# Performance work log

Measured on AMD Instinct MI355X. Metric: run time of the kernel, lower is better.

## Reference

```python
import jax, jax.numpy as jnp
import numpy as np

NE = 8192       # number of mesh elements
B = 64          # batch of density fields
AVG_DEG = 32    # neighbors per element within filter radius
NNZ = NE * AVG_DEG
NEG_SLOPE = 0.001


def setup_inputs() -> dict:
    key = jax.random.key(0)
    kx, kw, ks, ki = jax.random.split(key, 4)
    x = jax.random.normal(kx, (B, NE), dtype=jnp.float32)
    fc1_weight = jax.random.normal(kw, (NE, NE), dtype=jnp.float32) * (1.0 / np.sqrt(NE))
    # sparse weights initialized uniform(-bound, bound), bound = sqrt(2/Ne)
    bound = float(np.sqrt(2.0 / NE))
    sparse_weights = jax.random.uniform(ks, (NNZ,), dtype=jnp.float32,
                                        minval=-bound, maxval=bound)
    # static COO pattern (row, col) derived from mesh connectivity Rij < Rmin
    sparse_indices = jax.random.randint(ki, (2, NNZ), 0, NE, dtype=jnp.int64)
    return {"x": x, "fc1_weight": fc1_weight,
            "sparse_weights": sparse_weights, "sparse_indices": sparse_indices}


def reference(x, fc1_weight, sparse_weights, sparse_indices):
    # dense layer: h[b, i] = sum_k x[b, k] * W[i, k]
    h = x @ fc1_weight.T                         # [B, Ne]
    rows = sparse_indices[0]                     # [nnz]
    cols = sparse_indices[1]                     # [nnz]
    # sparse mm: out[b, j] = sum_{(i,j) in pattern} h[b, i] * w_{ij}
    contrib = h[:, rows] * sparse_weights        # [B, nnz] gather + scale
    out = jnp.zeros((x.shape[0], fc1_weight.shape[0]), dtype=h.dtype)
    out = out.at[:, cols].add(contrib)           # scatter-add over columns
    # leaky_relu, negative_slope = 0.001
    return jnp.where(out >= 0, out, NEG_SLOPE * out)
```

## Files before the change

kernel.cpp:

```cpp
#include <hip/hip_runtime.h>
#include <hip/hip_bf16.h>

#define NE 8192
#define BATCH 64
#define NNZT (NE * 32)
#define KSPLIT 4
#define KCH (NE / KSPLIT)
#define BK 128
#define NSTEP (KCH / BK)
#define TN 64

typedef float f32x2 __attribute__((ext_vector_type(2)));
typedef float f32x4 __attribute__((ext_vector_type(4)));
typedef short s16x8 __attribute__((ext_vector_type(8)));

__device__ __forceinline__ unsigned f2bf(float f) {
  unsigned u = __builtin_bit_cast(unsigned, f);
  return (u + 0x7FFFu + ((u >> 16) & 1u)) >> 16;
}

__global__ void k_convert_x(const float* __restrict__ x, unsigned short* __restrict__ xb) {
  int i = (blockIdx.x * 256 + threadIdx.x) * 4;
  float4 v = *reinterpret_cast<const float4*>(x + i);
  *reinterpret_cast<ushort4*>(xb + i) =
      make_ushort4((unsigned short)f2bf(v.x), (unsigned short)f2bf(v.y),
                   (unsigned short)f2bf(v.z), (unsigned short)f2bf(v.w));
}

__global__ void k_zero(float* __restrict__ p) {
  int i = (blockIdx.x * 256 + threadIdx.x) * 4;
  *reinterpret_cast<float4*>(p + i) = make_float4(0.f, 0.f, 0.f, 0.f);
}

__global__ __launch_bounds__(512, 4) void k_dense(const unsigned short* __restrict__ xb,
                                                  const float* __restrict__ W,
                                                  float* __restrict__ ht) {
  __shared__ __align__(16) char smem[65536];
  const int tid = threadIdx.x;
  const int wv = tid >> 6, l = tid & 63;
  const int kq = blockIdx.x & (KSPLIT - 1);
  const int i0 = (blockIdx.x >> 2) * TN;
  const int k0 = kq * KCH;

  const float* wsrc = W + (size_t)(i0 + wv * 8) * NE + k0 + l * 2;
  const unsigned short* xsrc = xb + (size_t)(wv * 8) * NE + k0 + l * 2;

  const int r16 = l & 15, q = l >> 4;
  const int wrow = (wv & 3) * 16 + r16;
  const int xrow0 = (wv >> 2) * 32 + r16;
  const int fxor = (r16 & 7) << 4;

  f32x4 acc0 = {}, acc1 = {};
  f32x2 wA[8], wB[8];
  unsigned xA[8], xB[8];

#define LOADW(WR, XR, s)                                                          \
  do {                                                                            \
    _Pragma("unroll") for (int j = 0; j < 8; ++j)                                 \
        WR[j] = *reinterpret_cast<const f32x2*>(wsrc + (size_t)j * NE + (s)*BK);  \
    _Pragma("unroll") for (int j = 0; j < 8; ++j)                                 \
        XR[j] = *reinterpret_cast<const unsigned*>(xsrc + (size_t)j * NE + (s)*BK); \
    __builtin_amdgcn_sched_barrier(0);                                            \
  } while (0)

#define STORE(WR, XR, buf)                                                        \
  do {                                                                            \
    _Pragma("unroll") for (int j = 0; j < 8; ++j) {                               \
      const int r_ = wv * 8 + j;                                                  \
      const int co_ = (l * 4) ^ ((r_ & 7) << 4);                                  \
      unsigned pw_ = f2bf(WR[j][0]) | (f2bf(WR[j][1]) << 16);                     \
      *reinterpret_cast<unsigned*>(smem + (buf)*16384 + r_ * 256 + co_) = pw_;    \
      *reinterpret_cast<unsigned*>(smem + 32768 + (buf)*16384 + r_ * 256 + co_) = XR[j]; \
    }                                                                             \
    __builtin_amdgcn_sched_barrier(0);                                            \
  } while (0)

#define COMPUTE(buf)                                                              \
  do {                                                                            \
    const char* wb_ = smem + (buf)*16384 + wrow * 256;                            \
    const char* xb0_ = smem + 32768 + (buf)*16384 + xrow0 * 256;                  \
    _Pragma("unroll") for (int ks = 0; ks < 4; ++ks) {                            \
      const int col_ = (ks * 64 + q * 16) ^ fxor;                                 \
      s16x8 bw_ = *reinterpret_cast<const s16x8*>(wb_ + col_);                    \
      s16x8 a0_ = *reinterpret_cast<const s16x8*>(xb0_ + col_);                   \
      s16x8 a1_ = *reinterpret_cast<const s16x8*>(xb0_ + 4096 + col_);            \
      acc0 = __builtin_amdgcn_mfma_f32_16x16x32_bf16(a0_, bw_, acc0, 0, 0, 0);    \
      acc1 = __builtin_amdgcn_mfma_f32_16x16x32_bf16(a1_, bw_, acc1, 0, 0, 0);    \
    }                                                                             \
    __builtin_amdgcn_sched_barrier(0);                                            \
  } while (0)

#define SBAR()                                              \
  do {                                                      \
    asm volatile("s_waitcnt lgkmcnt(0)" ::: "memory");      \
    __builtin_amdgcn_s_barrier();                           \
    __builtin_amdgcn_sched_barrier(0);                      \
  } while (0)

  LOADW(wA, xA, 0);
  LOADW(wB, xB, 1);
  STORE(wA, xA, 0);
  SBAR();

  for (int s = 0; s < NSTEP; s += 2) {
    if (s + 2 < NSTEP) LOADW(wA, xA, s + 2);
    if (s + 1 < NSTEP) STORE(wB, xB, 1);
    COMPUTE(0);
    SBAR();
    if (s + 3 < NSTEP) LOADW(wB, xB, s + 3);
    if (s + 2 < NSTEP) STORE(wA, xA, 0);
    COMPUTE(1);
    SBAR();
  }

#undef LOADW
#undef STORE
#undef COMPUTE
#undef SBAR

  float* hp = ht + (size_t)(i0 + wrow) * BATCH + (wv >> 2) * 32 + q * 4;
#pragma unroll
  for (int j = 0; j < 4; ++j) atomicAdd(hp + j, acc0[j]);
#pragma unroll
  for (int j = 0; j < 4; ++j) atomicAdd(hp + 16 + j, acc1[j]);
}

__global__ void k_scatter(const float* __restrict__ ht, const float* __restrict__ sw,
                          const int* __restrict__ rows, const int* __restrict__ cols,
                          float* __restrict__ out_t) {
  const int w = (blockIdx.x * 256 + threadIdx.x) >> 6;
  const int lane = threadIdx.x & 63;
  const int n0 = w * (NNZT / 4096);
#pragma unroll 4
  for (int n = n0; n < n0 + (NNZT / 4096); ++n) {
    const int r = rows[n];
    const int c = cols[n];
    const float wv = sw[n];
    atomicAdd(out_t + (size_t)c * BATCH + lane, ht[(size_t)r * BATCH + lane] * wv);
  }
}

__global__ void k_final(const float* __restrict__ out_t, float* __restrict__ out) {
  __shared__ float tile[64][65];
  const int t = threadIdx.x;
  const int j0 = blockIdx.x * 64;
  {
    const int jl = t >> 2, b0 = (t & 3) * 16;
    const float* src = out_t + (size_t)(j0 + jl) * BATCH + b0;
#pragma unroll
    for (int e = 0; e < 16; e += 4) {
      float4 v = *reinterpret_cast<const float4*>(src + e);
      tile[jl][b0 + e + 0] = v.x;
      tile[jl][b0 + e + 1] = v.y;
      tile[jl][b0 + e + 2] = v.z;
      tile[jl][b0 + e + 3] = v.w;
    }
  }
  __syncthreads();
  {
    const int bl = t >> 2, js = (t & 3) * 16;
    float* dst = out + (size_t)bl * NE + j0 + js;
#pragma unroll
    for (int e = 0; e < 16; e += 4) {
      float a0 = tile[js + e + 0][bl];
      float a1 = tile[js + e + 1][bl];
      float a2 = tile[js + e + 2][bl];
      float a3 = tile[js + e + 3][bl];
      float4 v;
      v.x = a0 >= 0.f ? a0 : 0.001f * a0;
      v.y = a1 >= 0.f ? a1 : 0.001f * a1;
      v.z = a2 >= 0.f ? a2 : 0.001f * a2;
      v.w = a3 >= 0.f ? a3 : 0.001f * a3;
      *reinterpret_cast<float4*>(dst + e) = v;
    }
  }
}

extern "C" void kernel_launch(void* const* d_in, const int* in_sizes, int n_in,
                              void* d_out, int out_size, void* d_ws, size_t ws_size,
                              hipStream_t stream) {
  const float* x = (const float*)d_in[0];
  const float* W = (const float*)d_in[1];
  const float* sw = (const float*)d_in[2];
  const int* idx = (const int*)d_in[3];
  float* out = (float*)d_out;

  char* ws = (char*)d_ws;
  float* ht = (float*)ws;
  float* out_t = (float*)(ws + (2 << 20));
  unsigned short* xbf = (unsigned short*)(ws + (4 << 20));

  k_convert_x<<<512, 256, 0, stream>>>(x, xbf);
  k_zero<<<1024, 256, 0, stream>>>((float*)ws);
  k_dense<<<512, 512, 0, stream>>>(xbf, W, ht);
  k_scatter<<<1024, 256, 0, stream>>>(ht, sw, idx, idx + NNZT, out_t);
  k_final<<<128, 256, 0, stream>>>(out_t, out);
}
```

Baseline: 137.4 us.

## Retile dense GEMM to 256-row tiles with 8-way K split

The dense bf16 MFMA kernel now gives each block 256 output rows over a 1024-wide K chunk with BK=64. Each wave computes a 32x64 tile with eight accumulators, so every x fragment read from shared memory is reused across more W rows. Global loads are widened to 16-byte vectors and the grid is halved to 256 blocks. The cost is more LDS per block (80KB) and more registers, which lowers occupancy to 2 blocks per CU, plus twice as many atomic adds into ht from the larger K split.

Result: slower. 166.2 us (+21.0%).

```diff
diff --git a/kernel.cpp b/kernel.cpp
--- a/kernel.cpp
+++ b/kernel.cpp
@@ -4,14 +4,15 @@
 #define NE 8192
 #define BATCH 64
 #define NNZT (NE * 32)
-#define KSPLIT 4
+#define KSPLIT 8
 #define KCH (NE / KSPLIT)
-#define BK 128
+#define BK 64
 #define NSTEP (KCH / BK)
-#define TN 64
-
-typedef float f32x2 __attribute__((ext_vector_type(2)));
+#define TN 256
+
 typedef float f32x4 __attribute__((ext_vector_type(4)));
+typedef unsigned u32x4 __attribute__((ext_vector_type(4)));
+typedef unsigned u32x2 __attribute__((ext_vector_type(2)));
 typedef short s16x8 __attribute__((ext_vector_type(8)));
 
 __device__ __forceinline__ unsigned f2bf(float f) {
@@ -32,62 +33,68 @@
   *reinterpret_cast<float4*>(p + i) = make_float4(0.f, 0.f, 0.f, 0.f);
 }
 
-__global__ __launch_bounds__(512, 4) void k_dense(const unsigned short* __restrict__ xb,
+__global__ __launch_bounds__(512, 2) void k_dense(const unsigned short* __restrict__ xb,
                                                   const float* __restrict__ W,
                                                   float* __restrict__ ht) {
-  __shared__ __align__(16) char smem[65536];
+  __shared__ __align__(16) char smem[81920];
   const int tid = threadIdx.x;
   const int wv = tid >> 6, l = tid & 63;
   const int kq = blockIdx.x & (KSPLIT - 1);
-  const int i0 = (blockIdx.x >> 2) * TN;
+  const int i0 = (blockIdx.x >> 3) * TN;
   const int k0 = kq * KCH;
 
-  const float* wsrc = W + (size_t)(i0 + wv * 8) * NE + k0 + l * 2;
-  const unsigned short* xsrc = xb + (size_t)(wv * 8) * NE + k0 + l * 2;
+  const float* wsrc = W + (size_t)(i0 + wv * 32 + (l >> 4)) * NE + k0 + (l & 15) * 4;
+  const unsigned short* xsrc = xb + (size_t)(wv * 8 + (l >> 3)) * NE + k0 + (l & 7) * 8;
 
   const int r16 = l & 15, q = l >> 4;
-  const int wrow = (wv & 3) * 16 + r16;
-  const int xrow0 = (wv >> 2) * 32 + r16;
   const int fxor = (r16 & 7) << 4;
-
-  f32x4 acc0 = {}, acc1 = {};
-  f32x2 wA[8], wB[8];
-  unsigned xA[8], xB[8];
-
-#define LOADW(WR, XR, s)                                                          \
-  do {                                                                            \
-    _Pragma("unroll") for (int j = 0; j < 8; ++j)                                 \
-        WR[j] = *reinterpret_cast<const f32x2*>(wsrc + (size_t)j * NE + (s)*BK);  \
-    _Pragma("unroll") for (int j = 0; j < 8; ++j)                                 \
-        XR[j] = *reinterpret_cast<const unsigned*>(xsrc + (size_t)j * NE + (s)*BK); \
-    __builtin_amdgcn_sched_barrier(0);                                            \
-  } while (0)
-
-#define STORE(WR, XR, buf)                                                        \
-  do {                                                                            \
-    _Pragma("unroll") for (int j = 0; j < 8; ++j) {                               \
-      const int r_ = wv * 8 + j;                                                  \
-      const int co_ = (l * 4) ^ ((r_ & 7) << 4);                                  \
-      unsigned pw_ = f2bf(WR[j][0]) | (f2bf(WR[j][1]) << 16);                     \
-      *reinterpret_cast<unsigned*>(smem + (buf)*16384 + r_ * 256 + co_) = pw_;    \
-      *reinterpret_cast<unsigned*>(smem + 32768 + (buf)*16384 + r_ * 256 + co_) = XR[j]; \
-    }                                                                             \
-    __builtin_amdgcn_sched_barrier(0);                                            \
-  } while (0)
-
-#define COMPUTE(buf)                                                              \
-  do {                                                                            \
-    const char* wb_ = smem + (buf)*16384 + wrow * 256;                            \
-    const char* xb0_ = smem + 32768 + (buf)*16384 + xrow0 * 256;                  \
-    _Pragma("unroll") for (int ks = 0; ks < 4; ++ks) {                            \
-      const int col_ = (ks * 64 + q * 16) ^ fxor;                                 \
-      s16x8 bw_ = *reinterpret_cast<const s16x8*>(wb_ + col_);                    \
-      s16x8 a0_ = *reinterpret_cast<const s16x8*>(xb0_ + col_);                   \
-      s16x8 a1_ = *reinterpret_cast<const s16x8*>(xb0_ + 4096 + col_);            \
-      acc0 = __builtin_amdgcn_mfma_f32_16x16x32_bf16(a0_, bw_, acc0, 0, 0, 0);    \
-      acc1 = __builtin_amdgcn_mfma_f32_16x16x32_bf16(a1_, bw_, acc1, 0, 0, 0);    \
-    }                                                                             \
-    __builtin_amdgcn_sched_barrier(0);                                            \
+  const int wrow0 = wv * 32 + r16;
+  const int wdr = wv * 32 + (l >> 4);
+  const int xdr = wv * 8 + (l >> 3);
+
+  f32x4 acc0[4] = {}, acc1[4] = {};
+  f32x4 wA[8], wB[8];
+  u32x4 xA, xB;
+
+#define LOADW(WR, XR, s)                                                           \
+  do {                                                                             \
+    _Pragma("unroll") for (int j = 0; j < 8; ++j)                                  \
+        WR[j] = *reinterpret_cast<const f32x4*>(wsrc + (size_t)j * 4 * NE + (s)*BK); \
+    XR = *reinterpret_cast<const u32x4*>(xsrc + (s)*BK);                           \
+    __builtin_amdgcn_sched_barrier(0);                                             \
+  } while (0)
+
+#define STORE(WR, XR, buf)                                                         \
+  do {                                                                             \
+    _Pragma("unroll") for (int j = 0; j < 8; ++j) {                                \
+      const int r_ = wdr + j * 4;                                                  \
+      const int co_ = ((l & 15) * 8) ^ ((r_ & 7) << 4);                            \
+      u32x2 pw_;                                                                   \
+      pw_[0] = f2bf(WR[j][0]) | (f2bf(WR[j][1]) << 16);                            \
+      pw_[1] = f2bf(WR[j][2]) | (f2bf(WR[j][3]) << 16);                            \
+      *reinterpret_cast<u32x2*>(smem + (buf)*32768 + r_ * 128 + co_) = pw_;        \
+    }                                                                              \
+    {                                                                              \
+      const int cx_ = ((l & 7) * 16) ^ ((xdr & 7) << 4);                           \
+      *reinterpret_cast<u32x4*>(smem + 65536 + (buf)*8192 + xdr * 128 + cx_) = XR; \
+    }                                                                              \
+    __builtin_amdgcn_sched_barrier(0);                                             \
+  } while (0)
+
+#define COMPUTE(buf)                                                               \
+  do {                                                                             \
+    _Pragma("unroll") for (int ks = 0; ks < 2; ++ks) {                             \
+      const int col_ = (ks * 64 + q * 16) ^ fxor;                                  \
+      s16x8 b0_ = *reinterpret_cast<const s16x8*>(smem + (buf)*32768 + wrow0 * 128 + col_); \
+      s16x8 b1_ = *reinterpret_cast<const s16x8*>(smem + (buf)*32768 + (wrow0 + 16) * 128 + col_); \
+      _Pragma("unroll") for (int g = 0; g < 4; ++g) {                              \
+        s16x8 a_ = *reinterpret_cast<const s16x8*>(smem + 65536 + (buf)*8192 +     \
+                                                   (g * 16 + r16) * 128 + col_);   \
+        acc0[g] = __builtin_amdgcn_mfma_f32_16x16x32_bf16(a_, b0_, acc0[g], 0, 0, 0); \
+        acc1[g] = __builtin_amdgcn_mfma_f32_16x16x32_bf16(a_, b1_, acc1[g], 0, 0, 0); \
+      }                                                                            \
+    }                                                                              \
+    __builtin_amdgcn_sched_barrier(0);                                             \
   } while (0)
 
 #define SBAR()                                              \
@@ -118,11 +125,16 @@
 #undef COMPUTE
 #undef SBAR
 
-  float* hp = ht + (size_t)(i0 + wrow) * BATCH + (wv >> 2) * 32 + q * 4;
-#pragma unroll
-  for (int j = 0; j < 4; ++j) atomicAdd(hp + j, acc0[j]);
-#pragma unroll
-  for (int j = 0; j < 4; ++j) atomicAdd(hp + 16 + j, acc1[j]);
+#pragma unroll
+  for (int g = 0; g < 4; ++g) {
+    float* hp0 = ht + (size_t)(i0 + wrow0) * BATCH + g * 16 + q * 4;
+    float* hp1 = ht + (size_t)(i0 + wrow0 + 16) * BATCH + g * 16 + q * 4;
+#pragma unroll
+    for (int j = 0; j < 4; ++j) {
+      atomicAdd(hp0 + j, acc0[g][j]);
+      atomicAdd(hp1 + j, acc1[g][j]);
+    }
+  }
 }
 
 __global__ void k_scatter(const float* __restrict__ ht, const float* __restrict__ sw,
@@ -192,7 +204,7 @@
 
   k_convert_x<<<512, 256, 0, stream>>>(x, xbf);
   k_zero<<<1024, 256, 0, stream>>>((float*)ws);
-  k_dense<<<512, 512, 0, stream>>>(xbf, W, ht);
+  k_dense<<<256, 512, 0, stream>>>(xbf, W, ht);
   k_scatter<<<1024, 256, 0, stream>>>(ht, sw, idx, idx + NNZT, out_t);
   k_final<<<128, 256, 0, stream>>>(out_t, out);
 }
```

## Shrink dense GEMM tiles to 32 rows, split K eight ways, 256-thread blocks

Applied to the files above, without the earlier changes.

Retiles the dense bf16 MFMA kernel. Each block now covers 32 output rows with 4 waves instead of 64 rows with 8 waves, the K dimension is split 8 ways instead of 4, and the K step drops from 128 to 64. This gives 2048 smaller blocks with less LDS each, aiming for more blocks per CU and better spread of the memory-bound weight streaming. The cost is more global atomic adds into h, more reloads of the x tiles, and narrower 4-byte W loads per lane.

New measurement: 165.4 us. +20.4%, slower.

```diff
diff --git a/kernel.cpp b/kernel.cpp
--- a/kernel.cpp
+++ b/kernel.cpp
@@ -4,13 +4,12 @@
 #define NE 8192
 #define BATCH 64
 #define NNZT (NE * 32)
-#define KSPLIT 4
+#define KSPLIT 8
 #define KCH (NE / KSPLIT)
-#define BK 128
+#define BK 64
 #define NSTEP (KCH / BK)
-#define TN 64
-
-typedef float f32x2 __attribute__((ext_vector_type(2)));
+#define TN 32
+
 typedef float f32x4 __attribute__((ext_vector_type(4)));
 typedef short s16x8 __attribute__((ext_vector_type(8)));
 
@@ -32,60 +31,61 @@
   *reinterpret_cast<float4*>(p + i) = make_float4(0.f, 0.f, 0.f, 0.f);
 }
 
-__global__ __launch_bounds__(512, 4) void k_dense(const unsigned short* __restrict__ xb,
+__global__ __launch_bounds__(256, 6) void k_dense(const unsigned short* __restrict__ xb,
                                                   const float* __restrict__ W,
                                                   float* __restrict__ ht) {
-  __shared__ __align__(16) char smem[65536];
+  __shared__ __align__(16) char smem[24576];
   const int tid = threadIdx.x;
   const int wv = tid >> 6, l = tid & 63;
   const int kq = blockIdx.x & (KSPLIT - 1);
-  const int i0 = (blockIdx.x >> 2) * TN;
+  const int i0 = (blockIdx.x >> 3) * TN;
   const int k0 = kq * KCH;
 
-  const float* wsrc = W + (size_t)(i0 + wv * 8) * NE + k0 + l * 2;
-  const unsigned short* xsrc = xb + (size_t)(wv * 8) * NE + k0 + l * 2;
+  const float* wsrc = W + (size_t)(i0 + wv * 8) * NE + k0 + l;
+  const unsigned short* xsrc = xb + (size_t)(wv * 16 + (l >> 5)) * NE + k0 + (l & 31) * 2;
 
   const int r16 = l & 15, q = l >> 4;
-  const int wrow = (wv & 3) * 16 + r16;
-  const int xrow0 = (wv >> 2) * 32 + r16;
   const int fxor = (r16 & 7) << 4;
 
   f32x4 acc0 = {}, acc1 = {};
-  f32x2 wA[8], wB[8];
+  float wA[8], wB[8];
   unsigned xA[8], xB[8];
 
 #define LOADW(WR, XR, s)                                                          \
   do {                                                                            \
     _Pragma("unroll") for (int j = 0; j < 8; ++j)                                 \
-        WR[j] = *reinterpret_cast<const f32x2*>(wsrc + (size_t)j * NE + (s)*BK);  \
+        WR[j] = *(wsrc + (size_t)j * NE + (s)*BK);                                \
     _Pragma("unroll") for (int j = 0; j < 8; ++j)                                 \
-        XR[j] = *reinterpret_cast<const unsigned*>(xsrc + (size_t)j * NE + (s)*BK); \
+        XR[j] = *reinterpret_cast<const unsigned*>(xsrc + (size_t)(2 * j) * NE + (s)*BK); \
     __builtin_amdgcn_sched_barrier(0);                                            \
   } while (0)
 
 #define STORE(WR, XR, buf)                                                        \
   do {                                                                            \
     _Pragma("unroll") for (int j = 0; j < 8; ++j) {                               \
-      const int r_ = wv * 8 + j;                                                  \
-      const int co_ = (l * 4) ^ ((r_ & 7) << 4);                                  \
-      unsigned pw_ = f2bf(WR[j][0]) | (f2bf(WR[j][1]) << 16);                     \
-      *reinterpret_cast<unsigned*>(smem + (buf)*16384 + r_ * 256 + co_) = pw_;    \
-      *reinterpret_cast<unsigned*>(smem + 32768 + (buf)*16384 + r_ * 256 + co_) = XR[j]; \
+      const int rw_ = wv * 8 + j;                                                 \
+      const int co_ = (l * 2) ^ ((rw_ & 7) << 4);                                 \
+      *reinterpret_cast<unsigned short*>(smem + (buf)*4096 + rw_ * 128 + co_) =   \
+          (unsigned short)f2bf(WR[j]);                                            \
+    }                                                                             \
+    _Pragma("unroll") for (int j = 0; j < 8; ++j) {                               \
+      const int rx_ = wv * 16 + 2 * j + (l >> 5);                                 \
+      const int cx_ = ((l & 31) * 4) ^ ((rx_ & 7) << 4);                          \
+      *reinterpret_cast<unsigned*>(smem + 8192 + (buf)*8192 + rx_ * 128 + cx_) = XR[j]; \
     }                                                                             \
     __builtin_amdgcn_sched_barrier(0);                                            \
   } while (0)
 
 #define COMPUTE(buf)                                                              \
   do {                                                                            \
-    const char* wb_ = smem + (buf)*16384 + wrow * 256;                            \
-    const char* xb0_ = smem + 32768 + (buf)*16384 + xrow0 * 256;                  \
-    _Pragma("unroll") for (int ks = 0; ks < 4; ++ks) {                            \
+    _Pragma("unroll") for (int ks = 0; ks < 2; ++ks) {                            \
       const int col_ = (ks * 64 + q * 16) ^ fxor;                                 \
-      s16x8 bw_ = *reinterpret_cast<const s16x8*>(wb_ + col_);                    \
-      s16x8 a0_ = *reinterpret_cast<const s16x8*>(xb0_ + col_);                   \
-      s16x8 a1_ = *reinterpret_cast<const s16x8*>(xb0_ + 4096 + col_);            \
-      acc0 = __builtin_amdgcn_mfma_f32_16x16x32_bf16(a0_, bw_, acc0, 0, 0, 0);    \
-      acc1 = __builtin_amdgcn_mfma_f32_16x16x32_bf16(a1_, bw_, acc1, 0, 0, 0);    \
+      s16x8 b0_ = *reinterpret_cast<const s16x8*>(smem + (buf)*4096 + r16 * 128 + col_); \
+      s16x8 b1_ = *reinterpret_cast<const s16x8*>(smem + (buf)*4096 + (16 + r16) * 128 + col_); \
+      s16x8 a_ = *reinterpret_cast<const s16x8*>(smem + 8192 + (buf)*8192 +       \
+                                                 (wv * 16 + r16) * 128 + col_);   \
+      acc0 = __builtin_amdgcn_mfma_f32_16x16x32_bf16(a_, b0_, acc0, 0, 0, 0);     \
+      acc1 = __builtin_amdgcn_mfma_f32_16x16x32_bf16(a_, b1_, acc1, 0, 0, 0);     \
     }                                                                             \
     __builtin_amdgcn_sched_barrier(0);                                            \
   } while (0)
@@ -118,11 +118,13 @@
 #undef COMPUTE
 #undef SBAR
 
-  float* hp = ht + (size_t)(i0 + wrow) * BATCH + (wv >> 2) * 32 + q * 4;
+  float* hp0 = ht + (size_t)(i0 + r16) * BATCH + wv * 16 + q * 4;
+  float* hp1 = ht + (size_t)(i0 + 16 + r16) * BATCH + wv * 16 + q * 4;
 #pragma unroll
-  for (int j = 0; j < 4; ++j) atomicAdd(hp + j, acc0[j]);
-#pragma unroll
-  for (int j = 0; j < 4; ++j) atomicAdd(hp + 16 + j, acc1[j]);
+  for (int j = 0; j < 4; ++j) {
+    atomicAdd(hp0 + j, acc0[j]);
+    atomicAdd(hp1 + j, acc1[j]);
+  }
 }
 
 __global__ void k_scatter(const float* __restrict__ ht, const float* __restrict__ sw,
@@ -192,7 +194,7 @@
 
   k_convert_x<<<512, 256, 0, stream>>>(x, xbf);
   k_zero<<<1024, 256, 0, stream>>>((float*)ws);
-  k_dense<<<512, 512, 0, stream>>>(xbf, W, ht);
+  k_dense<<<2048, 256, 0, stream>>>(xbf, W, ht);
   k_scatter<<<1024, 256, 0, stream>>>(ht, sw, idx, idx + NNZT, out_t);
   k_final<<<128, 256, 0, stream>>>(out_t, out);
 }
```
